# Kernel optimization log

Hardware: AMD Instinct MI355X
Metric: run time of the kernel (lower is better)

The kernel has to match this reference:

```python
import jax, jax.numpy as jnp
import numpy as np

HIDDEN = 128
NUM_HEADS = 8
F32_MIN = jnp.finfo(jnp.float32).min


def _split_heads(x, n):
    # [B, S, D] -> [B, n, S, D//n]
    b, s, d = x.shape
    return x.reshape(b, s, n, d // n).transpose(0, 2, 1, 3)


def setup_inputs() -> dict:
    key = jax.random.key(0)
    k1, k2, k3 = jax.random.split(key, 3)
    B, S = 4, 2048
    key_and_value = jax.random.normal(k1, (B, S, 2 * HIDDEN), dtype=jnp.float32)
    query = jax.random.normal(k2, (B, S, HIDDEN), dtype=jnp.float32)
    seq_len = jax.random.randint(k3, (B, 1), 1, S + 1, dtype=jnp.int32)
    return {"key_and_value": key_and_value, "query": query, "seq_len": seq_len}


def reference(key_and_value, query, seq_len):
    B, S, _ = query.shape
    d_head = HIDDEN // NUM_HEADS
    k, v = jnp.split(key_and_value, 2, axis=2)           # each [B, S, HIDDEN]
    Q = _split_heads(query, NUM_HEADS) * (d_head ** 0.5)  # NOTE: original MULTIPLIES by sqrt(d_head)
    K = _split_heads(k, NUM_HEADS)
    V = _split_heads(v, NUM_HEADS)
    # scores: [B, H, S, S]
    logits = jnp.einsum('bhqd,bhkd->bhqk', Q, K)
    # length mask over key positions: valid where pos < seq_len (one-hot+cumsum trick)
    valid = (jnp.arange(S, dtype=jnp.int32)[None, :] < seq_len).astype(jnp.float32)  # [B, S]
    logits = logits + F32_MIN * (1.0 - valid[:, None, None, :])
    weights = jax.nn.softmax(logits, axis=-1)
    out = jnp.einsum('bhqk,bhkd->bhqd', weights, V)       # [B, H, S, d_head]
    return out.transpose(0, 2, 1, 3).reshape(B, S, HIDDEN)
```

## Files before the change

### kernel.cpp

```cpp
#include <hip/hip_runtime.h>
#include <hip/hip_bf16.h>

#define HIDDEN 128
#define NHEAD  8
#define DHEAD  16
#define KBLK   64
#define QPB    2
#define TILEB  4096
#define QSCALE 5.77078016355585277626f

typedef __attribute__((ext_vector_type(8))) _Float16 f16x8;
typedef __attribute__((ext_vector_type(4))) _Float16 f16x4;
typedef __attribute__((ext_vector_type(4))) float  f32x4;
typedef __attribute__((ext_vector_type(2))) float  f32x2;
typedef __attribute__((ext_vector_type(4))) int    i32x4;

__device__ __forceinline__ int ksub(int k)  { return ((k >> 5) << 1) | ((k >> 2) & 1); }
__device__ __forceinline__ int kirow(int k) { return (((k >> 3) & 3) << 2) | (k & 3); }

__device__ __forceinline__ void cvt_store(char* Sb, int ka, i32x4 vaddr,
                                          f32x4 kvec, f32x4 vvec)
{
    f16x4 kh;
    #pragma unroll
    for (int i = 0; i < 4; ++i) kh[i] = (_Float16)kvec[i];
    *(f16x4*)(Sb + ka) = kh;
    #pragma unroll
    for (int i = 0; i < 4; ++i)
        *(_Float16*)(Sb + vaddr[i]) = (_Float16)vvec[i];
}

template<bool SPLIT>
__global__ __launch_bounds__(256, 4)
void mha_fwd(const float* __restrict__ kv,
             const float* __restrict__ q,
             const int*   __restrict__ seq_len,
             float* __restrict__ out,
             _Float16* __restrict__ pbuf,
             float* __restrict__ mlbuf,
             int S, int nc, int chunk)
{
    const int qpair = blockIdx.x;
    const int h     = blockIdx.y;
    int b, c0;
    if (SPLIT) { const int Bn = gridDim.z / nc; b = blockIdx.z % Bn; c0 = blockIdx.z / Bn; }
    else       { b = blockIdx.z; c0 = 0; }
    const int L = seq_len[b];
    const int kstart = SPLIT ? c0 * chunk : 0;
    if (SPLIT && kstart >= L) return;
    const int kend = SPLIT ? min(L, kstart + chunk) : L;

    const int tid  = threadIdx.x;
    const int lane = tid & 63;
    const int wave = tid >> 6;
    const int g    = lane >> 4;
    const int lr   = lane & 15;
    const int sw   = (lr & 7) << 4;

    __shared__ __align__(16) char Stg[2][TILEB];

    const int qrowb = qpair * (QPB * KBLK) + wave * 16 + lr;
    f16x8 qf[QPB];
    #pragma unroll
    for (int qt = 0; qt < QPB; ++qt) {
        const float* qp = q + ((size_t)(b * S + qrowb + qt * KBLK) * HIDDEN) + h * DHEAD + (g & 1) * 8;
        #pragma unroll
        for (int j = 0; j < 8; ++j) {
            float qv = qp[j] * QSCALE;
            _Float16 hi = (_Float16)qv;
            qf[qt][j] = (g < 2) ? hi : (_Float16)(qv - (float)hi);
        }
    }

    const int sk = tid >> 2;
    const int qd = tid & 3;
    const float* kvp = kv + ((size_t)(b * S + sk) * (2 * HIDDEN)) + h * DHEAD + 4 * qd;
    const int ka = ksub(sk) * 512 + (qd >> 1) * 256 + kirow(sk) * 16 + (qd & 1) * 8;
    i32x4 vaddr;
    #pragma unroll
    for (int i = 0; i < 4; ++i) {
        const int d = 4 * qd + i;
        vaddr[i] = 2048 + d * 128 + (((sk >> 3) * 16) ^ ((d & 7) << 4)) + (sk & 7) * 2;
    }

    f32x4 acc[QPB];
    float m[QPB], lsum[QPB];
    #pragma unroll
    for (int qt = 0; qt < QPB; ++qt) {
        acc[qt] = (f32x4){0.f, 0.f, 0.f, 0.f};
        m[qt] = -1e30f; lsum[qt] = 0.f;
    }

    const int ntiles = (kend - kstart + KBLK - 1) >> 6;

    {
        const float* kp = kvp + (size_t)kstart * (2 * HIDDEN);
        f32x4 kvec = *(const f32x4*)kp;
        f32x4 vvec = *(const f32x4*)(kp + HIDDEN);
        cvt_store(&Stg[0][0], ka, vaddr, kvec, vvec);
    }
    __syncthreads();

    for (int ti = 0; ti < ntiles; ++ti) {
        const int kb = kstart + ti * KBLK;
        const char* Sb = &Stg[ti & 1][0];
        const bool hasnext = (ti + 1) < ntiles;

        f32x4 nkv, nvv;
        if (hasnext) {
            const float* kp = kvp + (size_t)(kb + KBLK) * (2 * HIDDEN);
            nkv = *(const f32x4*)kp;
            nvv = *(const f32x4*)(kp + HIDDEN);
        }

        f16x8 kf[4];
        #pragma unroll
        for (int sub = 0; sub < 4; ++sub)
            kf[sub] = *(const f16x8*)(Sb + sub * 512 + (g & 1) * 256 + lr * 16);
        f16x8 vb0 = *(const f16x8*)(Sb + 2048 + lr * 128 + ((g * 16) ^ sw));
        f16x8 vb1 = *(const f16x8*)(Sb + 2048 + lr * 128 + ((64 + g * 16) ^ sw));

        const bool bnd = (kb + KBLK > kend);

        #pragma unroll
        for (int qt = 0; qt < QPB; ++qt) {
            f32x4 s[4];
            #pragma unroll
            for (int sub = 0; sub < 4; ++sub) {
                f32x4 z = {0.f, 0.f, 0.f, 0.f};
                s[sub] = __builtin_amdgcn_mfma_f32_16x16x32_f16(kf[sub], qf[qt], z, 0, 0, 0);
            }
            if (bnd) {
                #pragma unroll
                for (int sub = 0; sub < 4; ++sub) {
                    const int kb2 = kb + (sub >> 1) * 32 + (sub & 1) * 4 + g * 8;
                    #pragma unroll
                    for (int r = 0; r < 4; ++r)
                        if (kb2 + r >= kend) s[sub][r] = -1e30f;
                }
            }

            float t0 = fmaxf(fmaxf(s[0][0], s[0][1]), fmaxf(s[0][2], s[0][3]));
            float t1 = fmaxf(fmaxf(s[1][0], s[1][1]), fmaxf(s[1][2], s[1][3]));
            float t2 = fmaxf(fmaxf(s[2][0], s[2][1]), fmaxf(s[2][2], s[2][3]));
            float t3 = fmaxf(fmaxf(s[3][0], s[3][1]), fmaxf(s[3][2], s[3][3]));
            float tmax = fmaxf(fmaxf(t0, t1), fmaxf(t2, t3));
            tmax = fmaxf(tmax, __shfl_xor(tmax, 16));
            tmax = fmaxf(tmax, __shfl_xor(tmax, 32));

            const float mn = fmaxf(m[qt], tmax);
            const float alpha = exp2f(m[qt] - mn);
            m[qt] = mn;

            float rsum = 0.f;
            f16x8 pa0, pa1;
            #pragma unroll
            for (int sub = 0; sub < 2; ++sub)
                #pragma unroll
                for (int r = 0; r < 4; ++r) {
                    float p = exp2f(s[sub][r] - mn);
                    rsum += p;
                    pa0[sub * 4 + r] = (_Float16)p;
                }
            #pragma unroll
            for (int sub = 2; sub < 4; ++sub)
                #pragma unroll
                for (int r = 0; r < 4; ++r) {
                    float p = exp2f(s[sub][r] - mn);
                    rsum += p;
                    pa1[(sub - 2) * 4 + r] = (_Float16)p;
                }
            rsum += __shfl_xor(rsum, 16);
            rsum += __shfl_xor(rsum, 32);
            lsum[qt] = lsum[qt] * alpha + rsum;
            acc[qt] *= alpha;

            acc[qt] = __builtin_amdgcn_mfma_f32_16x16x32_f16(vb0, pa0, acc[qt], 0, 0, 0);
            acc[qt] = __builtin_amdgcn_mfma_f32_16x16x32_f16(vb1, pa1, acc[qt], 0, 0, 0);
        }

        if (hasnext)
            cvt_store(&Stg[(ti + 1) & 1][0], ka, vaddr, nkv, nvv);
        __syncthreads();
    }

    #pragma unroll
    for (int qt = 0; qt < QPB; ++qt) {
        const int qglob = qrowb + qt * KBLK;
        if (SPLIT) {
            const size_t row = (((size_t)b * nc + c0) * S + qglob) * NHEAD + h;
            f16x4 pk;
            #pragma unroll
            for (int r = 0; r < 4; ++r) pk[r] = (_Float16)acc[qt][r];
            *(f16x4*)&pbuf[row * DHEAD + g * 4] = pk;
            if (g == 0) { f32x2 ml = {m[qt], lsum[qt]}; *(f32x2*)&mlbuf[row * 2] = ml; }
        } else {
            const float inv = 1.0f / lsum[qt];
            *(f32x4*)&out[((size_t)b * S + qglob) * HIDDEN + h * DHEAD + g * 4] = acc[qt] * inv;
        }
    }
}

__global__ __launch_bounds__(256)
void mha_merge(const _Float16* __restrict__ pbuf, const float* __restrict__ mlbuf,
               const int* __restrict__ seq_len, float* __restrict__ out,
               int S, int nc, int chunk)
{
    const int t = blockIdx.x * 256 + threadIdx.x;
    const int h = t & (NHEAD - 1);
    const int rest = t >> 3;
    const int qg = rest % S;
    const int b  = rest / S;
    const int L  = seq_len[b];
    const int nch = min(nc, (L + chunk - 1) / chunk);

    const size_t cstr = (size_t)S * NHEAD;
    const size_t row0 = ((size_t)b * nc) * cstr + (size_t)qg * NHEAD + h;

    float mv[8], lv[8];
    float M = -1e30f;
    for (int c = 0; c < nch; ++c) {
        f32x2 ml = *(const f32x2*)&mlbuf[(row0 + c * cstr) * 2];
        mv[c] = ml[0]; lv[c] = ml[1];
        M = fmaxf(M, ml[0]);
    }
    float den = 0.f;
    float o[16];
    #pragma unroll
    for (int i = 0; i < 16; ++i) o[i] = 0.f;
    for (int c = 0; c < nch; ++c) {
        float w = exp2f(mv[c] - M);
        den += w * lv[c];
        const _Float16* pp = &pbuf[(row0 + c * cstr) * DHEAD];
        f16x8 p0 = *(const f16x8*)&pp[0];
        f16x8 p1 = *(const f16x8*)&pp[8];
        #pragma unroll
        for (int i = 0; i < 8; ++i) {
            o[i]     += w * (float)p0[i];
            o[i + 8] += w * (float)p1[i];
        }
    }
    const float inv = 1.0f / den;
    float* op = &out[((size_t)b * S + qg) * HIDDEN + h * DHEAD];
    #pragma unroll
    for (int i = 0; i < 4; ++i) {
        f32x4 v = {o[4*i] * inv, o[4*i+1] * inv, o[4*i+2] * inv, o[4*i+3] * inv};
        *(f32x4*)&op[4 * i] = v;
    }
}

extern "C" void kernel_launch(void* const* d_in, const int* in_sizes, int n_in,
                              void* d_out, int out_size, void* d_ws, size_t ws_size,
                              hipStream_t stream)
{
    const float* kv      = (const float*)d_in[0];
    const float* query   = (const float*)d_in[1];
    const int*   seq_len = (const int*)d_in[2];
    float* out           = (float*)d_out;

    const int B = in_sizes[2];
    const int S = in_sizes[1] / (B * HIDDEN);

    const int chunk = 512;
    const int nc = (S + chunk - 1) / chunk;
    const size_t mlb = (size_t)B * nc * S * NHEAD * 2 * sizeof(float);
    const size_t pbb = (size_t)B * nc * S * NHEAD * DHEAD * sizeof(_Float16);

    if (nc <= 8 && ws_size >= mlb + pbb) {
        float* mlbuf = (float*)d_ws;
        _Float16* pbuf = (_Float16*)((char*)d_ws + mlb);
        mha_fwd<true><<<dim3(S / (QPB * KBLK), NHEAD, B * nc), dim3(256), 0, stream>>>(
            kv, query, seq_len, nullptr, pbuf, mlbuf, S, nc, chunk);
        const int nrows = B * S * NHEAD;
        mha_merge<<<dim3((nrows + 255) / 256), dim3(256), 0, stream>>>(
            pbuf, mlbuf, seq_len, out, S, nc, chunk);
    } else {
        mha_fwd<false><<<dim3(S / (QPB * KBLK), NHEAD, B), dim3(256), 0, stream>>>(
            kv, query, seq_len, out, nullptr, nullptr, S, 1, S);
    }
}
```

Measured before the change: 40.33 us.

## Batch MFMAs across query tiles, raise priority, defer row-sum reduction

Restructures the inner loop so that the score MFMAs for all query tiles are issued together, then softmax runs for each tile, then the PV MFMAs are issued together. s_setprio is raised around the MFMA groups. The per-tile cross-lane reduction of the partial row sum is moved out of the loop into a single reduction after it. The aim is better MFMA/VALU interleaving and fewer shuffles, at the cost of higher register pressure from holding all score tiles at once.

Measured after the change: 38.54 us, median of 3. -4.4%, faster.

```diff
diff --git a/kernel.cpp b/kernel.cpp
--- a/kernel.cpp
+++ b/kernel.cpp
@@ -122,28 +122,36 @@
 
         const bool bnd = (kb + KBLK > kend);
 
-        #pragma unroll
-        for (int qt = 0; qt < QPB; ++qt) {
-            f32x4 s[4];
+        f32x4 s[QPB][4];
+        __builtin_amdgcn_s_setprio(1);
+        #pragma unroll
+        for (int qt = 0; qt < QPB; ++qt)
             #pragma unroll
             for (int sub = 0; sub < 4; ++sub) {
                 f32x4 z = {0.f, 0.f, 0.f, 0.f};
-                s[sub] = __builtin_amdgcn_mfma_f32_16x16x32_f16(kf[sub], qf[qt], z, 0, 0, 0);
+                s[qt][sub] = __builtin_amdgcn_mfma_f32_16x16x32_f16(kf[sub], qf[qt], z, 0, 0, 0);
             }
-            if (bnd) {
+        __builtin_amdgcn_s_setprio(0);
+
+        if (bnd) {
+            #pragma unroll
+            for (int qt = 0; qt < QPB; ++qt)
                 #pragma unroll
                 for (int sub = 0; sub < 4; ++sub) {
                     const int kb2 = kb + (sub >> 1) * 32 + (sub & 1) * 4 + g * 8;
                     #pragma unroll
                     for (int r = 0; r < 4; ++r)
-                        if (kb2 + r >= kend) s[sub][r] = -1e30f;
+                        if (kb2 + r >= kend) s[qt][sub][r] = -1e30f;
                 }
-            }
-
-            float t0 = fmaxf(fmaxf(s[0][0], s[0][1]), fmaxf(s[0][2], s[0][3]));
-            float t1 = fmaxf(fmaxf(s[1][0], s[1][1]), fmaxf(s[1][2], s[1][3]));
-            float t2 = fmaxf(fmaxf(s[2][0], s[2][1]), fmaxf(s[2][2], s[2][3]));
-            float t3 = fmaxf(fmaxf(s[3][0], s[3][1]), fmaxf(s[3][2], s[3][3]));
+        }
+
+        f16x8 pa[QPB][2];
+        #pragma unroll
+        for (int qt = 0; qt < QPB; ++qt) {
+            float t0 = fmaxf(fmaxf(s[qt][0][0], s[qt][0][1]), fmaxf(s[qt][0][2], s[qt][0][3]));
+            float t1 = fmaxf(fmaxf(s[qt][1][0], s[qt][1][1]), fmaxf(s[qt][1][2], s[qt][1][3]));
+            float t2 = fmaxf(fmaxf(s[qt][2][0], s[qt][2][1]), fmaxf(s[qt][2][2], s[qt][2][3]));
+            float t3 = fmaxf(fmaxf(s[qt][3][0], s[qt][3][1]), fmaxf(s[qt][3][2], s[qt][3][3]));
             float tmax = fmaxf(fmaxf(t0, t1), fmaxf(t2, t3));
             tmax = fmaxf(tmax, __shfl_xor(tmax, 16));
             tmax = fmaxf(tmax, __shfl_xor(tmax, 32));
@@ -153,31 +161,25 @@
             m[qt] = mn;
 
             float rsum = 0.f;
-            f16x8 pa0, pa1;
-            #pragma unroll
-            for (int sub = 0; sub < 2; ++sub)
+            #pragma unroll
+            for (int sub = 0; sub < 4; ++sub)
                 #pragma unroll
                 for (int r = 0; r < 4; ++r) {
-                    float p = exp2f(s[sub][r] - mn);
+                    float p = exp2f(s[qt][sub][r] - mn);
                     rsum += p;
-                    pa0[sub * 4 + r] = (_Float16)p;
+                    pa[qt][sub >> 1][(sub & 1) * 4 + r] = (_Float16)p;
                 }
-            #pragma unroll
-            for (int sub = 2; sub < 4; ++sub)
-                #pragma unroll
-                for (int r = 0; r < 4; ++r) {
-                    float p = exp2f(s[sub][r] - mn);
-                    rsum += p;
-                    pa1[(sub - 2) * 4 + r] = (_Float16)p;
-                }
-            rsum += __shfl_xor(rsum, 16);
-            rsum += __shfl_xor(rsum, 32);
             lsum[qt] = lsum[qt] * alpha + rsum;
             acc[qt] *= alpha;
-
-            acc[qt] = __builtin_amdgcn_mfma_f32_16x16x32_f16(vb0, pa0, acc[qt], 0, 0, 0);
-            acc[qt] = __builtin_amdgcn_mfma_f32_16x16x32_f16(vb1, pa1, acc[qt], 0, 0, 0);
-        }
+        }
+
+        __builtin_amdgcn_s_setprio(1);
+        #pragma unroll
+        for (int qt = 0; qt < QPB; ++qt) {
+            acc[qt] = __builtin_amdgcn_mfma_f32_16x16x32_f16(vb0, pa[qt][0], acc[qt], 0, 0, 0);
+            acc[qt] = __builtin_amdgcn_mfma_f32_16x16x32_f16(vb1, pa[qt][1], acc[qt], 0, 0, 0);
+        }
+        __builtin_amdgcn_s_setprio(0);
 
         if (hasnext)
             cvt_store(&Stg[(ti + 1) & 1][0], ka, vaddr, nkv, nvv);
@@ -186,6 +188,8 @@
 
     #pragma unroll
     for (int qt = 0; qt < QPB; ++qt) {
+        lsum[qt] += __shfl_xor(lsum[qt], 16);
+        lsum[qt] += __shfl_xor(lsum[qt], 32);
         const int qglob = qrowb + qt * KBLK;
         if (SPLIT) {
             const size_t row = (((size_t)b * nc + c0) * S + qglob) * NHEAD + h;
```
